# Optimization experiments

Hardware: AMD Instinct MI355X
Metric: run time of the kernel (lower is better)

Reference implementation:

```python
import jax, jax.numpy as jnp
import numpy as np

B, S = 256, 32          # sequence layout for the final (b, s, 1) reshape
BATCH = B * S           # 8192 flattened rows processed per call
IN, U, OUT = 32, 128, 1 # sensory inputs, interneurons, motor outputs
UNFOLDS = 6             # semi-implicit ODE solver unfolds


def _syn_sigmoid(v, mu, sigma):
    # v: [B, P]; mu, sigma: [P, Q] -> [B, P, Q] per-synapse gate
    return jax.nn.sigmoid(sigma * (v[:, :, None] - mu))


def setup_inputs() -> dict:
    key = jax.random.key(0)
    ks = jax.random.split(key, 12)
    inputs = jax.random.normal(ks[0], (BATCH, IN), dtype=jnp.float32)
    state = jax.random.normal(ks[1], (BATCH, U), dtype=jnp.float32)
    # adjacency in {-1, 0, 1} (wiring polarity), baked into W / erev as in _get_variables
    sens_adj = jax.random.randint(ks[2], (IN, U), -1, 2).astype(jnp.float32)
    adj = jax.random.randint(ks[3], (U, U), -1, 2).astype(jnp.float32)
    sensory_mu = jax.random.uniform(ks[4], (IN, U)) * 0.5 + 0.3
    sensory_sigma = jax.random.uniform(ks[5], (IN, U)) * 5.0 + 3.0
    # NOTE: original applies +w_init_min OUTSIDE the |adj| mask; reproduced faithfully
    sensory_W = jnp.abs(sens_adj) * jax.random.uniform(ks[6], (IN, U)) * 0.9 + 0.1
    sensory_erev = sens_adj  # erev_init_factor = 1
    mu = jax.random.uniform(ks[7], (U, U)) * 0.5 + 0.3
    sigma = jax.random.uniform(ks[8], (U, U)) * 5.0 + 3.0
    W = jnp.abs(adj) * jax.random.uniform(ks[9], (U, U)) * 0.9 + 0.1
    erev = adj
    vleak = jax.random.uniform(ks[10], (U,)) * 0.4 - 0.2
    gleak = jnp.ones((U,), jnp.float32)        # gleak_init_min == gleak_init_max == 1
    cm_t = jnp.ones((U,), jnp.float32) * 0.5    # cm_init_min == cm_init_max == 0.5
    in_w = jnp.ones((IN,), jnp.float32)         # affine input mapping (init ones/zeros)
    in_b = jnp.zeros((IN,), jnp.float32)
    out_w = jnp.ones((OUT,), jnp.float32)       # affine output mapping
    out_b = jnp.zeros((OUT,), jnp.float32)
    return dict(inputs=inputs, state=state, sensory_mu=sensory_mu,
                sensory_sigma=sensory_sigma, sensory_W=sensory_W,
                sensory_erev=sensory_erev, mu=mu, sigma=sigma, W=W, erev=erev,
                vleak=vleak, gleak=gleak, cm_t=cm_t, in_w=in_w, in_b=in_b,
                out_w=out_w, out_b=out_b, b=B, s=S)


def reference(inputs, state, sensory_mu, sensory_sigma, sensory_W, sensory_erev,
              mu, sigma, W, erev, vleak, gleak, cm_t, in_w, in_b, out_w, out_b,
              b, s):
    x = inputs * in_w + in_b                                   # _map_inputs (Affine)
    # sensory synapse activations, computed once: [BATCH, IN, U]
    sa = sensory_W * _syn_sigmoid(x, sensory_mu, sensory_sigma)
    w_num_s = jnp.sum(sa * sensory_erev, axis=1)               # [BATCH, U]
    w_den_s = jnp.sum(sa, axis=1)                              # [BATCH, U]

    def step(v, _):
        wa = W * _syn_sigmoid(v, mu, sigma)                    # [BATCH, U, U]
        w_num = jnp.sum(wa * erev, axis=1) + w_num_s
        w_den = jnp.sum(wa, axis=1) + w_den_s
        v_new = (cm_t * v + gleak * vleak + w_num) / (cm_t + gleak + w_den)
        return v_new, None

    v, _ = jax.lax.scan(step, state, None, length=UNFOLDS)
    outputs = (v[:, :OUT] * out_w + out_b).reshape(b, s, 1)    # _map_outputs
    return outputs, v
```

## Files before the change

### kernel.cpp

```cpp
#include <hip/hip_runtime.h>

#define NIN 32
#define NU  128
#define RPB 8
#define UNFOLDS 6
#define LOG2E 1.44269504088896340736f

__global__ __launch_bounds__(256, 4)
void wormnet_kernel(const float* __restrict__ inputs,
                    const float* __restrict__ state,
                    const float* __restrict__ smu,
                    const float* __restrict__ ssig,
                    const float* __restrict__ sW,
                    const float* __restrict__ serev,
                    const float* __restrict__ rmu,
                    const float* __restrict__ rsig,
                    const float* __restrict__ rW,
                    const float* __restrict__ rerev,
                    const float* __restrict__ vleak,
                    const float* __restrict__ gleak,
                    const float* __restrict__ cm_t,
                    const float* __restrict__ in_w,
                    const float* __restrict__ in_b,
                    const float* __restrict__ out_w,
                    const float* __restrict__ out_b,
                    float* __restrict__ out_y,
                    float* __restrict__ out_v)
{
    __shared__ float xs[NIN * RPB];
    __shared__ float vs[NU * RPB];
    __shared__ float num1[NU * RPB];
    __shared__ float den1[NU * RPB];

    const int tid  = threadIdx.x;
    const int j    = tid & (NU - 1);
    const int h    = tid >> 7;
    const int base = blockIdx.x * RPB;

    {
        int i = tid & (NIN - 1);
        int r = tid >> 5;
        float x = inputs[(base + r) * NIN + i] * in_w[i] + in_b[i];
        xs[i * RPB + r] = x;
    }
    {
        int jj = tid & (NU - 1);
        int rr = tid >> 7;
        #pragma unroll
        for (int k = 0; k < 4; ++k) {
            int r = rr + 2 * k;
            vs[jj * RPB + r] = state[(base + r) * NU + jj];
        }
    }
    __syncthreads();

    float numS[RPB], denS[RPB];
    #pragma unroll
    for (int r = 0; r < RPB; ++r) { numS[r] = 0.0f; denS[r] = 0.0f; }
    {
        const int i0 = h * (NIN / 2);
        #pragma unroll 2
        for (int ii = 0; ii < NIN / 2; ++ii) {
            const int i = i0 + ii;
            const float m  = smu [i * NU + j];
            const float sg = ssig[i * NU + j];
            const float Wv = sW  [i * NU + j];
            const float er = serev[i * NU + j];
            const float s2  = -LOG2E * sg;
            const float sm2 = -s2 * m;
            const float We  = Wv * er;
            #pragma unroll
            for (int r = 0; r < RPB; ++r) {
                float t = __builtin_fmaf(s2, xs[i * RPB + r], sm2);
                float e = __builtin_amdgcn_exp2f(t);
                float sgm = __builtin_amdgcn_rcpf(1.0f + e);
                numS[r] = __builtin_fmaf(We, sgm, numS[r]);
                denS[r] = __builtin_fmaf(Wv, sgm, denS[r]);
            }
        }
    }

    float cm = 0.0f, glvl = 0.0f, cg = 0.0f;
    float vold[RPB];
    #pragma unroll
    for (int r = 0; r < RPB; ++r) vold[r] = 0.0f;
    if (h == 0) {
        cm = cm_t[j];
        float gl = gleak[j];
        glvl = gl * vleak[j];
        cg = cm + gl;
        #pragma unroll
        for (int r = 0; r < RPB; ++r) vold[r] = vs[j * RPB + r];
    }

    for (int u = 0; u < UNFOLDS; ++u) {
        float num[RPB], den[RPB];
        #pragma unroll
        for (int r = 0; r < RPB; ++r) { num[r] = numS[r]; den[r] = denS[r]; }

        const int i0 = h * (NU / 2);
        #pragma unroll 2
        for (int ii = 0; ii < NU / 2; ++ii) {
            const int i = i0 + ii;
            const float m  = rmu [i * NU + j];
            const float sg = rsig[i * NU + j];
            const float Wv = rW  [i * NU + j];
            const float er = rerev[i * NU + j];
            const float s2  = -LOG2E * sg;
            const float sm2 = -s2 * m;
            const float We  = Wv * er;
            #pragma unroll
            for (int r = 0; r < RPB; ++r) {
                float t = __builtin_fmaf(s2, vs[i * RPB + r], sm2);
                float e = __builtin_amdgcn_exp2f(t);
                float sgm = __builtin_amdgcn_rcpf(1.0f + e);
                num[r] = __builtin_fmaf(We, sgm, num[r]);
                den[r] = __builtin_fmaf(Wv, sgm, den[r]);
            }
        }

        if (h == 1) {
            #pragma unroll
            for (int r = 0; r < RPB; ++r) {
                num1[j * RPB + r] = num[r];
                den1[j * RPB + r] = den[r];
            }
        }
        __syncthreads();
        if (h == 0) {
            #pragma unroll
            for (int r = 0; r < RPB; ++r) {
                float tn = num[r] + num1[j * RPB + r];
                float td = den[r] + den1[j * RPB + r];
                float vn = (__builtin_fmaf(cm, vold[r], glvl) + tn)
                           * __builtin_amdgcn_rcpf(cg + td);
                vold[r] = vn;
                vs[j * RPB + r] = vn;
            }
        }
        __syncthreads();
    }

    if (h == 0) {
        #pragma unroll
        for (int r = 0; r < RPB; ++r) {
            out_v[(base + r) * NU + j] = vold[r];
        }
        if (j == 0) {
            const float ow = out_w[0], ob = out_b[0];
            #pragma unroll
            for (int r = 0; r < RPB; ++r) {
                out_y[base + r] = vold[r] * ow + ob;
            }
        }
    }
}

extern "C" void kernel_launch(void* const* d_in, const int* in_sizes, int n_in,
                              void* d_out, int out_size, void* d_ws, size_t ws_size,
                              hipStream_t stream) {
    const float* inputs  = (const float*)d_in[0];
    const float* state   = (const float*)d_in[1];
    const float* smu     = (const float*)d_in[2];
    const float* ssig    = (const float*)d_in[3];
    const float* sW      = (const float*)d_in[4];
    const float* serev   = (const float*)d_in[5];
    const float* rmu     = (const float*)d_in[6];
    const float* rsig    = (const float*)d_in[7];
    const float* rW      = (const float*)d_in[8];
    const float* rerev   = (const float*)d_in[9];
    const float* vleak   = (const float*)d_in[10];
    const float* gleak   = (const float*)d_in[11];
    const float* cm_t    = (const float*)d_in[12];
    const float* in_w    = (const float*)d_in[13];
    const float* in_b    = (const float*)d_in[14];
    const float* out_w   = (const float*)d_in[15];
    const float* out_b   = (const float*)d_in[16];

    const int batch = in_sizes[1] / NU;
    float* out_y = (float*)d_out;
    float* out_v = (float*)d_out + batch;

    dim3 grid(batch / RPB), block(256);
    hipLaunchKernelGGL(wormnet_kernel, grid, block, 0, stream,
                       inputs, state, smu, ssig, sW, serev,
                       rmu, rsig, rW, rerev, vleak, gleak, cm_t,
                       in_w, in_b, out_w, out_b, out_y, out_v);
}
```

Before: 284.5 us.

## Split rows across half-blocks and pack synapse params into float4 workspace

Before, the two 128-thread halves split the input-neuron reduction and combined partial sums through shared memory with two barriers per unfold. Now each half owns four of the eight rows and loops over all inputs, which removes the cross-half reduction and keeps one barrier per unfold by double-buffering the voltage array. A pre-pass kernel packs mu/sigma/W/erev into precomputed float4 tuples in the workspace, so each synapse becomes one vector load instead of four loads plus arithmetic. Shared-memory reads become float4 vector loads. The cost is two extra small kernel launches per call, and each thread now does twice the parameter loads per row processed.

```diff
diff --git a/kernel.cpp b/kernel.cpp
--- a/kernel.cpp
+++ b/kernel.cpp
@@ -3,155 +3,157 @@
 #define NIN 32
 #define NU  128
 #define RPB 8
+#define RPT 4
 #define UNFOLDS 6
 #define LOG2E 1.44269504088896340736f
 
+typedef float float4v __attribute__((ext_vector_type(4)));
+
+#define SPN (NIN * NU)
+#define RPN (NU * NU)
+
+__global__ void pack_params(const float* __restrict__ mu,
+                            const float* __restrict__ sig,
+                            const float* __restrict__ W,
+                            const float* __restrict__ erev,
+                            float4v* __restrict__ out, int n) {
+    int idx = blockIdx.x * blockDim.x + threadIdx.x;
+    if (idx < n) {
+        float sg = sig[idx];
+        float s2 = -LOG2E * sg;
+        float sm2 = -s2 * mu[idx];
+        float Wv = W[idx];
+        float We = Wv * erev[idx];
+        out[idx] = (float4v){s2, sm2, We, Wv};
+    }
+}
+
+template <bool PACKED>
 __global__ __launch_bounds__(256, 4)
-void wormnet_kernel(const float* __restrict__ inputs,
-                    const float* __restrict__ state,
-                    const float* __restrict__ smu,
-                    const float* __restrict__ ssig,
-                    const float* __restrict__ sW,
-                    const float* __restrict__ serev,
-                    const float* __restrict__ rmu,
-                    const float* __restrict__ rsig,
-                    const float* __restrict__ rW,
-                    const float* __restrict__ rerev,
-                    const float* __restrict__ vleak,
-                    const float* __restrict__ gleak,
-                    const float* __restrict__ cm_t,
-                    const float* __restrict__ in_w,
-                    const float* __restrict__ in_b,
-                    const float* __restrict__ out_w,
-                    const float* __restrict__ out_b,
-                    float* __restrict__ out_y,
-                    float* __restrict__ out_v)
+void wormnet_main(const float* __restrict__ inputs,
+                  const float* __restrict__ state,
+                  const float4v* __restrict__ sp,
+                  const float4v* __restrict__ rp,
+                  const float* __restrict__ smu, const float* __restrict__ ssig,
+                  const float* __restrict__ sW,  const float* __restrict__ serev,
+                  const float* __restrict__ rmu, const float* __restrict__ rsig,
+                  const float* __restrict__ rW,  const float* __restrict__ rerev,
+                  const float* __restrict__ vleak,
+                  const float* __restrict__ gleak,
+                  const float* __restrict__ cm_t,
+                  const float* __restrict__ in_w, const float* __restrict__ in_b,
+                  const float* __restrict__ out_w, const float* __restrict__ out_b,
+                  float* __restrict__ out_y,
+                  float* __restrict__ out_v)
 {
-    __shared__ float xs[NIN * RPB];
-    __shared__ float vs[NU * RPB];
-    __shared__ float num1[NU * RPB];
-    __shared__ float den1[NU * RPB];
+    __shared__ __align__(16) float xs[NIN * RPB];
+    __shared__ __align__(16) float vs[2][NU * RPB];
 
     const int tid  = threadIdx.x;
     const int j    = tid & (NU - 1);
-    const int h    = tid >> 7;
+    const int rh   = tid >> 7;
+    const int r0   = rh * RPT;
     const int base = blockIdx.x * RPB;
 
     {
         int i = tid & (NIN - 1);
         int r = tid >> 5;
-        float x = inputs[(base + r) * NIN + i] * in_w[i] + in_b[i];
-        xs[i * RPB + r] = x;
+        xs[i * RPB + r] = inputs[(base + r) * NIN + i] * in_w[i] + in_b[i];
     }
     {
-        int jj = tid & (NU - 1);
-        int rr = tid >> 7;
         #pragma unroll
         for (int k = 0; k < 4; ++k) {
-            int r = rr + 2 * k;
-            vs[jj * RPB + r] = state[(base + r) * NU + jj];
+            int r = rh + 2 * k;
+            vs[0][j * RPB + r] = state[(base + r) * NU + j];
         }
     }
     __syncthreads();
 
-    float numS[RPB], denS[RPB];
+    float numS[RPT], denS[RPT];
     #pragma unroll
-    for (int r = 0; r < RPB; ++r) { numS[r] = 0.0f; denS[r] = 0.0f; }
-    {
-        const int i0 = h * (NIN / 2);
-        #pragma unroll 2
-        for (int ii = 0; ii < NIN / 2; ++ii) {
-            const int i = i0 + ii;
-            const float m  = smu [i * NU + j];
-            const float sg = ssig[i * NU + j];
-            const float Wv = sW  [i * NU + j];
-            const float er = serev[i * NU + j];
-            const float s2  = -LOG2E * sg;
-            const float sm2 = -s2 * m;
-            const float We  = Wv * er;
+    for (int r = 0; r < RPT; ++r) { numS[r] = 0.0f; denS[r] = 0.0f; }
+
+    #pragma unroll 4
+    for (int i = 0; i < NIN; ++i) {
+        float4v p;
+        if (PACKED) {
+            p = sp[i * NU + j];
+        } else {
+            int idx = i * NU + j;
+            float sg = ssig[idx];
+            float s2 = -LOG2E * sg;
+            p = (float4v){s2, -s2 * smu[idx], sW[idx] * serev[idx], sW[idx]};
+        }
+        float4v xv = *(const float4v*)&xs[i * RPB + r0];
+        #pragma unroll
+        for (int r = 0; r < RPT; ++r) {
+            float t = __builtin_fmaf(p.x, xv[r], p.y);
+            float e = __builtin_amdgcn_exp2f(t);
+            float sgm = __builtin_amdgcn_rcpf(1.0f + e);
+            numS[r] = __builtin_fmaf(p.z, sgm, numS[r]);
+            denS[r] = __builtin_fmaf(p.w, sgm, denS[r]);
+        }
+    }
+
+    const float cm = cm_t[j];
+    const float gl = gleak[j];
+    const float glvl = gl * vleak[j];
+    const float cg = cm + gl;
+    float vold[RPT];
+    #pragma unroll
+    for (int r = 0; r < RPT; ++r) vold[r] = vs[0][j * RPB + r0 + r];
+
+    int cur = 0;
+    for (int u = 0; u < UNFOLDS; ++u) {
+        float num[RPT], den[RPT];
+        #pragma unroll
+        for (int r = 0; r < RPT; ++r) { num[r] = numS[r]; den[r] = denS[r]; }
+
+        #pragma unroll 4
+        for (int i = 0; i < NU; ++i) {
+            float4v p;
+            if (PACKED) {
+                p = rp[i * NU + j];
+            } else {
+                int idx = i * NU + j;
+                float sg = rsig[idx];
+                float s2 = -LOG2E * sg;
+                p = (float4v){s2, -s2 * rmu[idx], rW[idx] * rerev[idx], rW[idx]};
+            }
+            float4v vv = *(const float4v*)&vs[cur][i * RPB + r0];
             #pragma unroll
-            for (int r = 0; r < RPB; ++r) {
-                float t = __builtin_fmaf(s2, xs[i * RPB + r], sm2);
+            for (int r = 0; r < RPT; ++r) {
+                float t = __builtin_fmaf(p.x, vv[r], p.y);
                 float e = __builtin_amdgcn_exp2f(t);
                 float sgm = __builtin_amdgcn_rcpf(1.0f + e);
-                numS[r] = __builtin_fmaf(We, sgm, numS[r]);
-                denS[r] = __builtin_fmaf(Wv, sgm, denS[r]);
+                num[r] = __builtin_fmaf(p.z, sgm, num[r]);
+                den[r] = __builtin_fmaf(p.w, sgm, den[r]);
             }
         }
-    }
-
-    float cm = 0.0f, glvl = 0.0f, cg = 0.0f;
-    float vold[RPB];
+
+        float4v vnew;
+        #pragma unroll
+        for (int r = 0; r < RPT; ++r) {
+            float tn = __builtin_fmaf(cm, vold[r], glvl) + num[r];
+            float td = cg + den[r];
+            float vn = tn * __builtin_amdgcn_rcpf(td);
+            vold[r] = vn;
+            vnew[r] = vn;
+        }
+        *(float4v*)&vs[cur ^ 1][j * RPB + r0] = vnew;
+        __syncthreads();
+        cur ^= 1;
+    }
+
     #pragma unroll
-    for (int r = 0; r < RPB; ++r) vold[r] = 0.0f;
-    if (h == 0) {
-        cm = cm_t[j];
-        float gl = gleak[j];
-        glvl = gl * vleak[j];
-        cg = cm + gl;
-        #pragma unroll
-        for (int r = 0; r < RPB; ++r) vold[r] = vs[j * RPB + r];
-    }
-
-    for (int u = 0; u < UNFOLDS; ++u) {
-        float num[RPB], den[RPB];
-        #pragma unroll
-        for (int r = 0; r < RPB; ++r) { num[r] = numS[r]; den[r] = denS[r]; }
-
-        const int i0 = h * (NU / 2);
-        #pragma unroll 2
-        for (int ii = 0; ii < NU / 2; ++ii) {
-            const int i = i0 + ii;
-            const float m  = rmu [i * NU + j];
-            const float sg = rsig[i * NU + j];
-            const float Wv = rW  [i * NU + j];
-            const float er = rerev[i * NU + j];
-            const float s2  = -LOG2E * sg;
-            const float sm2 = -s2 * m;
-            const float We  = Wv * er;
-            #pragma unroll
-            for (int r = 0; r < RPB; ++r) {
-                float t = __builtin_fmaf(s2, vs[i * RPB + r], sm2);
-                float e = __builtin_amdgcn_exp2f(t);
-                float sgm = __builtin_amdgcn_rcpf(1.0f + e);
-                num[r] = __builtin_fmaf(We, sgm, num[r]);
-                den[r] = __builtin_fmaf(Wv, sgm, den[r]);
-            }
-        }
-
-        if (h == 1) {
-            #pragma unroll
-            for (int r = 0; r < RPB; ++r) {
-                num1[j * RPB + r] = num[r];
-                den1[j * RPB + r] = den[r];
-            }
-        }
-        __syncthreads();
-        if (h == 0) {
-            #pragma unroll
-            for (int r = 0; r < RPB; ++r) {
-                float tn = num[r] + num1[j * RPB + r];
-                float td = den[r] + den1[j * RPB + r];
-                float vn = (__builtin_fmaf(cm, vold[r], glvl) + tn)
-                           * __builtin_amdgcn_rcpf(cg + td);
-                vold[r] = vn;
-                vs[j * RPB + r] = vn;
-            }
-        }
-        __syncthreads();
-    }
-
-    if (h == 0) {
-        #pragma unroll
-        for (int r = 0; r < RPB; ++r) {
-            out_v[(base + r) * NU + j] = vold[r];
-        }
-        if (j == 0) {
-            const float ow = out_w[0], ob = out_b[0];
-            #pragma unroll
-            for (int r = 0; r < RPB; ++r) {
-                out_y[base + r] = vold[r] * ow + ob;
-            }
+    for (int r = 0; r < RPT; ++r) {
+        out_v[(base + r0 + r) * NU + j] = vold[r];
+    }
+    if (j == 0) {
+        const float ow = out_w[0], ob = out_b[0];
+        #pragma unroll
+        for (int r = 0; r < RPT; ++r) {
+            out_y[base + r0 + r] = __builtin_fmaf(vold[r], ow, ob);
         }
     }
 }
@@ -181,9 +183,30 @@
     float* out_y = (float*)d_out;
     float* out_v = (float*)d_out + batch;
 
+    const size_t need = (size_t)(SPN + RPN) * sizeof(float4v);
+    const bool packed = ws_size >= need;
+    float4v* sp = (float4v*)d_ws;
+    float4v* rp = sp + SPN;
+
+    if (packed) {
+        hipLaunchKernelGGL(pack_params, dim3((SPN + 255) / 256), dim3(256), 0, stream,
+                           smu, ssig, sW, serev, sp, SPN);
+        hipLaunchKernelGGL(pack_params, dim3((RPN + 255) / 256), dim3(256), 0, stream,
+                           rmu, rsig, rW, rerev, rp, RPN);
+    }
+
     dim3 grid(batch / RPB), block(256);
-    hipLaunchKernelGGL(wormnet_kernel, grid, block, 0, stream,
-                       inputs, state, smu, ssig, sW, serev,
-                       rmu, rsig, rW, rerev, vleak, gleak, cm_t,
-                       in_w, in_b, out_w, out_b, out_y, out_v);
+    if (packed) {
+        hipLaunchKernelGGL((wormnet_main<true>), grid, block, 0, stream,
+                           inputs, state, sp, rp,
+                           smu, ssig, sW, serev, rmu, rsig, rW, rerev,
+                           vleak, gleak, cm_t, in_w, in_b, out_w, out_b,
+                           out_y, out_v);
+    } else {
+        hipLaunchKernelGGL((wormnet_main<false>), grid, block, 0, stream,
+                           inputs, state, sp, rp,
+                           smu, ssig, sW, serev, rmu, rsig, rW, rerev,
+                           vleak, gleak, cm_t, in_w, in_b, out_w, out_b,
+                           out_y, out_v);
+    }
 }
```

After: 277.8 us. 2.4% less time.
